# Optimization experiments

Hardware: AMD Instinct MI355X
Metric: run time of the kernel (lower is better)

Reference implementation:

```python
import jax, jax.numpy as jnp
import numpy as np

EPS = 2.220446049250313e-16  # sys.float_info.epsilon
H_BW = 0.1  # bandwidth h


def setup_inputs() -> dict:
    key = jax.random.key(0)
    k1, k2 = jax.random.split(key)
    X = jax.random.normal(k1, (4, 256, 64, 64), dtype=jnp.float32)
    Y = jax.random.normal(k2, (4, 256, 64, 64), dtype=jnp.float32)
    return {"X_features": X, "Y_features": Y}


def _l2_normalize_c(f):
    # torch.norm(f, 2, dim=1, keepdim=True) + eps over channel dim of NCHW
    n = jnp.sqrt(jnp.sum(f * f, axis=1, keepdims=True)) + EPS
    return f / n


def reference(X_features, Y_features):
    B, C = X_features.shape[0], X_features.shape[1]
    # PONO centering: mean over channel dim of Y
    y_mean = jnp.mean(Y_features, axis=1, keepdims=True)  # [B,1,H,W]
    X = X_features - y_mean
    Y = Y_features - y_mean
    Xn = _l2_normalize_c(X).reshape(B, C, -1)  # [B,C,M]
    Yn = _l2_normalize_c(Y).reshape(B, C, -1)  # [B,C,M]
    # cosine distance matrix [B,M,M]
    d = 1.0 - jnp.einsum('bci,bcj->bij', Xn, Yn)
    d_norm = d / (jnp.min(d, axis=-1, keepdims=True) + 0.001)
    w = jnp.exp((1.0 - d_norm) / H_BW)
    A_ij = w / jnp.sum(w, axis=-1, keepdims=True)
    CX = jnp.mean(jnp.max(A_ij, axis=-1), axis=1)  # [B]
    return jnp.mean(-jnp.log(CX))
```

## Files before the change

kernel.cpp:

```cpp
#include <hip/hip_runtime.h>
#include <hip/hip_bf16.h>

typedef unsigned short u16;
typedef unsigned int u32;
typedef __attribute__((ext_vector_type(8))) __bf16 bf16x8;
typedef __attribute__((ext_vector_type(4))) float f32x4;
typedef __attribute__((ext_vector_type(8))) short short8;

#define EPSF 2.220446049250313e-16f

__device__ __forceinline__ u16 f2bf(float f) {
    u32 u = __float_as_uint(f);
    return (u16)((u + 0x7FFFu + ((u >> 16) & 1u)) >> 16);
}

__global__ __launch_bounds__(256) void prep_kernel(
    const float* __restrict__ X, const float* __restrict__ Y,
    u16* __restrict__ Xp, u16* __restrict__ Yp)
{
    const int blk = blockIdx.x;
    const int b = blk >> 8;
    const int fbase = blk & 255;
    const int t = threadIdx.x;
    const int px = t & 15, cg = t >> 4;
    const int l = t & 63, wv = t >> 6;
    const size_t base = (size_t)b * 256 * 4096 + (fbase << 4) + px;

    __shared__ float pA[4][16], pB[4][16];
    __shared__ float meanL[16], rnL[16];

    const int ks = cg >> 1;
    const int g0 = (cg & 1) << 1;
    const size_t pbase = (size_t)b << 20;
    const size_t addr0 = pbase + ((size_t)(fbase * 8 + ks) * 64 + g0 * 16 + px) * 8;

    float vals[16];

    {
        float s1 = 0.f, s2 = 0.f;
        #pragma unroll
        for (int k = 0; k < 16; ++k) {
            float v = Y[base + (size_t)(cg * 16 + k) * 4096];
            vals[k] = v; s1 += v; s2 += v * v;
        }
        s1 += __shfl_xor(s1, 16, 64); s2 += __shfl_xor(s2, 16, 64);
        s1 += __shfl_xor(s1, 32, 64); s2 += __shfl_xor(s2, 32, 64);
        if (l < 16) { pA[wv][l] = s1; pB[wv][l] = s2; }
        __syncthreads();
        if (t < 16) {
            float Sy = pA[0][t] + pA[1][t] + pA[2][t] + pA[3][t];
            float Syy = pB[0][t] + pB[1][t] + pB[2][t] + pB[3][t];
            float m = Sy * (1.f / 256.f);
            meanL[t] = m;
            rnL[t] = 1.f / (sqrtf(fmaxf(Syy - m * Sy, 0.f)) + EPSF);
        }
        __syncthreads();
        float m = meanL[px], rn = rnL[px];
        short8 h0, h1;
        #pragma unroll
        for (int k = 0; k < 8; ++k) {
            h0[k] = (short)f2bf((vals[k] - m) * rn);
            h1[k] = (short)f2bf((vals[8 + k] - m) * rn);
        }
        *(short8*)(Yp + addr0) = h0;
        *(short8*)(Yp + addr0 + 128) = h1;
        __syncthreads();
    }
    {
        float s1 = 0.f, s2 = 0.f;
        #pragma unroll
        for (int k = 0; k < 16; ++k) {
            float v = X[base + (size_t)(cg * 16 + k) * 4096];
            vals[k] = v; s1 += v; s2 += v * v;
        }
        s1 += __shfl_xor(s1, 16, 64); s2 += __shfl_xor(s2, 16, 64);
        s1 += __shfl_xor(s1, 32, 64); s2 += __shfl_xor(s2, 32, 64);
        if (l < 16) { pA[wv][l] = s1; pB[wv][l] = s2; }
        __syncthreads();
        if (t < 16) {
            float Sx = pA[0][t] + pA[1][t] + pA[2][t] + pA[3][t];
            float Sxx = pB[0][t] + pB[1][t] + pB[2][t] + pB[3][t];
            float m = meanL[t];
            rnL[t] = 1.f / (sqrtf(fmaxf(Sxx - 2.f * m * Sx + 256.f * m * m, 0.f)) + EPSF);
        }
        __syncthreads();
        float m = meanL[px], rn = rnL[px];
        short8 h0, h1;
        #pragma unroll
        for (int k = 0; k < 8; ++k) {
            h0[k] = (short)f2bf((vals[k] - m) * rn);
            h1[k] = (short)f2bf((vals[8 + k] - m) * rn);
        }
        *(short8*)(Xp + addr0) = h0;
        *(short8*)(Xp + addr0 + 128) = h1;
    }
}

template <int PASS>
__global__ __launch_bounds__(256, 2) void cx_pass(
    const u16* __restrict__ Xp, const u16* __restrict__ Yp,
    const float* __restrict__ partIn, float* __restrict__ partOut)
{
    __shared__ float smxL[64];
    __shared__ float redL[64][4];

    const int t = threadIdx.x;
    const int w = t >> 6, l = t & 63;
    const int l15 = l & 15, g = l >> 4;
    const int wc = w;

    const int id = blockIdx.x;
    const int xcd = id & 7, slot = id >> 3;
    const int b = xcd >> 1;
    const int it2 = ((xcd & 1) << 5) | (slot >> 1);
    const int jh = slot & 1;
    const int i0 = it2 << 6;

    const size_t pb = (size_t)b << 20;

    if (PASS == 1) {
        if (t < 64) {
            float2 v = ((const float2*)partIn)[(size_t)b * 4096 + i0 + t];
            smxL[t] = fmaxf(v.x, v.y);
        }
        __syncthreads();
    }

    bf16x8 a[4][8];
    {
        const u16* Apl = Xp + pb + (size_t)l * 8;
        #pragma unroll
        for (int fm = 0; fm < 4; ++fm)
            #pragma unroll
            for (int ks = 0; ks < 8; ++ks)
                a[fm][ks] = *(const bf16x8*)(Apl + (size_t)(((i0 >> 4) + fm) * 8 + ks) * 512);
    }

    float mo[4][4], it_[4][4];
    if (PASS == 1) {
        #pragma unroll
        for (int fm = 0; fm < 4; ++fm)
            #pragma unroll
            for (int r = 0; r < 4; ++r) {
                float m = smxL[fm * 16 + g * 4 + r];
                float iv = 14.4269504089f / (1.001f - m);
                it_[fm][r] = iv;
                mo[fm][r] = m * iv;
            }
    }

    float racc[4][4];
    #pragma unroll
    for (int fm = 0; fm < 4; ++fm)
        #pragma unroll
        for (int r = 0; r < 4; ++r) racc[fm][r] = (PASS == 0) ? -2.0f : 0.0f;

    const u16* Bpl = Yp + pb + (size_t)l * 8 + (size_t)(jh * 128 + wc) * 4096;
    #pragma unroll 1
    for (int u = 0; u < 32; ++u) {
        const u16* bp = Bpl + (size_t)u * 16384;
        f32x4 acc0 = {}, acc1 = {}, acc2 = {}, acc3 = {};
        #pragma unroll
        for (int ks = 0; ks < 8; ++ks) {
            bf16x8 bv = *(const bf16x8*)(bp + (ks << 9));
            acc0 = __builtin_amdgcn_mfma_f32_16x16x32_bf16(a[0][ks], bv, acc0, 0, 0, 0);
            acc1 = __builtin_amdgcn_mfma_f32_16x16x32_bf16(a[1][ks], bv, acc1, 0, 0, 0);
            acc2 = __builtin_amdgcn_mfma_f32_16x16x32_bf16(a[2][ks], bv, acc2, 0, 0, 0);
            acc3 = __builtin_amdgcn_mfma_f32_16x16x32_bf16(a[3][ks], bv, acc3, 0, 0, 0);
        }
        if (PASS == 0) {
            #pragma unroll
            for (int r = 0; r < 4; ++r) {
                racc[0][r] = fmaxf(racc[0][r], acc0[r]);
                racc[1][r] = fmaxf(racc[1][r], acc1[r]);
                racc[2][r] = fmaxf(racc[2][r], acc2[r]);
                racc[3][r] = fmaxf(racc[3][r], acc3[r]);
            }
        } else {
            #pragma unroll
            for (int r = 0; r < 4; ++r) {
                racc[0][r] += exp2f(__builtin_fmaf(acc0[r], it_[0][r], -mo[0][r]));
                racc[1][r] += exp2f(__builtin_fmaf(acc1[r], it_[1][r], -mo[1][r]));
                racc[2][r] += exp2f(__builtin_fmaf(acc2[r], it_[2][r], -mo[2][r]));
                racc[3][r] += exp2f(__builtin_fmaf(acc3[r], it_[3][r], -mo[3][r]));
            }
        }
    }

    #pragma unroll
    for (int fm = 0; fm < 4; ++fm)
        #pragma unroll
        for (int r = 0; r < 4; ++r) {
            float v = racc[fm][r];
            if (PASS == 0) {
                v = fmaxf(v, __shfl_xor(v, 1, 64));
                v = fmaxf(v, __shfl_xor(v, 2, 64));
                v = fmaxf(v, __shfl_xor(v, 4, 64));
                v = fmaxf(v, __shfl_xor(v, 8, 64));
            } else {
                v += __shfl_xor(v, 1, 64);
                v += __shfl_xor(v, 2, 64);
                v += __shfl_xor(v, 4, 64);
                v += __shfl_xor(v, 8, 64);
            }
            if (l15 == 0) redL[fm * 16 + g * 4 + r][wc] = v;
        }
    __syncthreads();
    if (t < 64) {
        float4 vv = *(const float4*)&redL[t][0];
        float res = (PASS == 0)
            ? fmaxf(fmaxf(vv.x, vv.y), fmaxf(vv.z, vv.w))
            : (vv.x + vv.y) + (vv.z + vv.w);
        partOut[((size_t)b * 4096 + i0 + t) * 2 + jh] = res;
    }
}

__global__ __launch_bounds__(256) void csum_kernel(
    const float* __restrict__ p1, float* __restrict__ csum)
{
    __shared__ float rr[4];
    const int t = threadIdx.x;
    const int row = blockIdx.x * 256 + t;
    float2 v = ((const float2*)p1)[row];
    float cx = 1.0f / (v.x + v.y);
    #pragma unroll
    for (int sh = 1; sh <= 32; sh <<= 1) cx += __shfl_xor(cx, sh, 64);
    if ((t & 63) == 0) rr[t >> 6] = cx;
    __syncthreads();
    if (t == 0) csum[blockIdx.x] = rr[0] + rr[1] + rr[2] + rr[3];
}

__global__ __launch_bounds__(64) void final_kernel(
    const float* __restrict__ csum, float* __restrict__ out)
{
    __shared__ float rb[4];
    const int t = threadIdx.x;
    float v = csum[t];
    v += __shfl_xor(v, 1, 64);
    v += __shfl_xor(v, 2, 64);
    v += __shfl_xor(v, 4, 64);
    v += __shfl_xor(v, 8, 64);
    if ((t & 15) == 0) rb[t >> 4] = v;
    __syncthreads();
    if (t == 0) {
        float loss = 0.f;
        #pragma unroll
        for (int bb = 0; bb < 4; ++bb)
            loss += -logf(rb[bb] * (1.f / 4096.f));
        out[0] = loss * 0.25f;
    }
}

extern "C" void kernel_launch(void* const* d_in, const int* in_sizes, int n_in,
                              void* d_out, int out_size, void* d_ws, size_t ws_size,
                              hipStream_t stream)
{
    const float* X = (const float*)d_in[0];
    const float* Y = (const float*)d_in[1];
    char* ws = (char*)d_ws;
    u16* Xp = (u16*)(ws);
    u16* Yp = (u16*)(ws + (8u << 20));
    float* part0 = (float*)(ws + (16u << 20));
    float* part1 = (float*)(ws + (16u << 20) + (128u << 10));
    float* csum  = (float*)(ws + (16u << 20) + (256u << 10));
    float* out = (float*)d_out;

    hipLaunchKernelGGL(prep_kernel, dim3(1024), dim3(256), 0, stream,
                       X, Y, Xp, Yp);
    hipLaunchKernelGGL((cx_pass<0>), dim3(512), dim3(256), 0, stream,
                       Xp, Yp, part0, part0);
    hipLaunchKernelGGL((cx_pass<1>), dim3(512), dim3(256), 0, stream,
                       Xp, Yp, part0, part1);
    hipLaunchKernelGGL(csum_kernel, dim3(64), dim3(256), 0, stream,
                       part1, csum);
    hipLaunchKernelGGL(final_kernel, dim3(1), dim3(64), 0, stream,
                       csum, out);
}
```

Before: 169.5 us.

## Shrink cx_pass tiles to 32 rows with 4-way column split; widen prep blocks

The cx_pass kernels now give each block 32 query rows and a quarter of the columns instead of 64 rows and half the columns. That launches 2048 blocks instead of 512, and launch bounds now request 4 blocks per SM, for higher occupancy and better latency hiding. The cost is less A-operand reuse per B load, so more B traffic, and more partial results to merge, with csum and pass 1 reading four partials per row. The prep kernel also moves to 512-thread blocks covering 32 pixels, reducing channel sums through shared memory instead of shuffles.

```diff
diff --git a/kernel.cpp b/kernel.cpp
--- a/kernel.cpp
+++ b/kernel.cpp
@@ -14,53 +14,51 @@
     return (u16)((u + 0x7FFFu + ((u >> 16) & 1u)) >> 16);
 }
 
-__global__ __launch_bounds__(256) void prep_kernel(
+__global__ __launch_bounds__(512) void prep_kernel(
     const float* __restrict__ X, const float* __restrict__ Y,
     u16* __restrict__ Xp, u16* __restrict__ Yp)
 {
     const int blk = blockIdx.x;
-    const int b = blk >> 8;
-    const int fbase = blk & 255;
-    const int t = threadIdx.x;
-    const int px = t & 15, cg = t >> 4;
-    const int l = t & 63, wv = t >> 6;
-    const size_t base = (size_t)b * 256 * 4096 + (fbase << 4) + px;
-
-    __shared__ float pA[4][16], pB[4][16];
-    __shared__ float meanL[16], rnL[16];
-
-    const int ks = cg >> 1;
-    const int g0 = (cg & 1) << 1;
+    const int b = blk >> 7;
+    const int p0 = (blk & 127) << 5;
+    const int t = threadIdx.x;
+    const int pxl = t & 31, cg = t >> 5;
+    const size_t base = (size_t)b * 256 * 4096 + p0 + pxl;
+
+    __shared__ float pS[16][32], pSS[16][32];
+    __shared__ float meanL[32], rnL[32];
+
     const size_t pbase = (size_t)b << 20;
-    const size_t addr0 = pbase + ((size_t)(fbase * 8 + ks) * 64 + g0 * 16 + px) * 8;
+    const int fb = (p0 + pxl) >> 4;
+    const int ks = cg >> 1, g0 = (cg & 1) << 1;
+    const size_t addr0 = pbase + ((size_t)(fb * 8 + ks) * 64 + g0 * 16 + (pxl & 15)) * 8;
 
     float vals[16];
 
     {
         float s1 = 0.f, s2 = 0.f;
         #pragma unroll
-        for (int k = 0; k < 16; ++k) {
-            float v = Y[base + (size_t)(cg * 16 + k) * 4096];
-            vals[k] = v; s1 += v; s2 += v * v;
-        }
-        s1 += __shfl_xor(s1, 16, 64); s2 += __shfl_xor(s2, 16, 64);
-        s1 += __shfl_xor(s1, 32, 64); s2 += __shfl_xor(s2, 32, 64);
-        if (l < 16) { pA[wv][l] = s1; pB[wv][l] = s2; }
-        __syncthreads();
-        if (t < 16) {
-            float Sy = pA[0][t] + pA[1][t] + pA[2][t] + pA[3][t];
-            float Syy = pB[0][t] + pB[1][t] + pB[2][t] + pB[3][t];
+        for (int e = 0; e < 16; ++e) {
+            float v = Y[base + (size_t)(cg * 16 + e) * 4096];
+            vals[e] = v; s1 += v; s2 += v * v;
+        }
+        pS[cg][pxl] = s1; pSS[cg][pxl] = s2;
+        __syncthreads();
+        if (t < 32) {
+            float Sy = 0.f, Syy = 0.f;
+            #pragma unroll
+            for (int c = 0; c < 16; ++c) { Sy += pS[c][t]; Syy += pSS[c][t]; }
             float m = Sy * (1.f / 256.f);
             meanL[t] = m;
             rnL[t] = 1.f / (sqrtf(fmaxf(Syy - m * Sy, 0.f)) + EPSF);
         }
         __syncthreads();
-        float m = meanL[px], rn = rnL[px];
+        const float m = meanL[pxl], rn = rnL[pxl];
         short8 h0, h1;
         #pragma unroll
-        for (int k = 0; k < 8; ++k) {
-            h0[k] = (short)f2bf((vals[k] - m) * rn);
-            h1[k] = (short)f2bf((vals[8 + k] - m) * rn);
+        for (int e = 0; e < 8; ++e) {
+            h0[e] = (short)f2bf((vals[e] - m) * rn);
+            h1[e] = (short)f2bf((vals[8 + e] - m) * rn);
         }
         *(short8*)(Yp + addr0) = h0;
         *(short8*)(Yp + addr0 + 128) = h1;
@@ -69,27 +67,26 @@
     {
         float s1 = 0.f, s2 = 0.f;
         #pragma unroll
-        for (int k = 0; k < 16; ++k) {
-            float v = X[base + (size_t)(cg * 16 + k) * 4096];
-            vals[k] = v; s1 += v; s2 += v * v;
-        }
-        s1 += __shfl_xor(s1, 16, 64); s2 += __shfl_xor(s2, 16, 64);
-        s1 += __shfl_xor(s1, 32, 64); s2 += __shfl_xor(s2, 32, 64);
-        if (l < 16) { pA[wv][l] = s1; pB[wv][l] = s2; }
-        __syncthreads();
-        if (t < 16) {
-            float Sx = pA[0][t] + pA[1][t] + pA[2][t] + pA[3][t];
-            float Sxx = pB[0][t] + pB[1][t] + pB[2][t] + pB[3][t];
+        for (int e = 0; e < 16; ++e) {
+            float v = X[base + (size_t)(cg * 16 + e) * 4096];
+            vals[e] = v; s1 += v; s2 += v * v;
+        }
+        pS[cg][pxl] = s1; pSS[cg][pxl] = s2;
+        __syncthreads();
+        if (t < 32) {
+            float Sx = 0.f, Sxx = 0.f;
+            #pragma unroll
+            for (int c = 0; c < 16; ++c) { Sx += pS[c][t]; Sxx += pSS[c][t]; }
             float m = meanL[t];
             rnL[t] = 1.f / (sqrtf(fmaxf(Sxx - 2.f * m * Sx + 256.f * m * m, 0.f)) + EPSF);
         }
         __syncthreads();
-        float m = meanL[px], rn = rnL[px];
+        const float m = meanL[pxl], rn = rnL[pxl];
         short8 h0, h1;
         #pragma unroll
-        for (int k = 0; k < 8; ++k) {
-            h0[k] = (short)f2bf((vals[k] - m) * rn);
-            h1[k] = (short)f2bf((vals[8 + k] - m) * rn);
+        for (int e = 0; e < 8; ++e) {
+            h0[e] = (short)f2bf((vals[e] - m) * rn);
+            h1[e] = (short)f2bf((vals[8 + e] - m) * rn);
         }
         *(short8*)(Xp + addr0) = h0;
         *(short8*)(Xp + addr0 + 128) = h1;
@@ -97,12 +94,12 @@
 }
 
 template <int PASS>
-__global__ __launch_bounds__(256, 2) void cx_pass(
+__global__ __launch_bounds__(256, 4) void cx_pass(
     const u16* __restrict__ Xp, const u16* __restrict__ Yp,
     const float* __restrict__ partIn, float* __restrict__ partOut)
 {
-    __shared__ float smxL[64];
-    __shared__ float redL[64][4];
+    __shared__ float smxL[32];
+    __shared__ float redL[32][4];
 
     const int t = threadIdx.x;
     const int w = t >> 6, l = t & 63;
@@ -112,34 +109,34 @@
     const int id = blockIdx.x;
     const int xcd = id & 7, slot = id >> 3;
     const int b = xcd >> 1;
-    const int it2 = ((xcd & 1) << 5) | (slot >> 1);
-    const int jh = slot & 1;
-    const int i0 = it2 << 6;
+    const int tl = ((xcd & 1) << 8) | slot;
+    const int it = tl >> 2, jq = tl & 3;
+    const int i0 = it << 5;
 
     const size_t pb = (size_t)b << 20;
 
     if (PASS == 1) {
-        if (t < 64) {
-            float2 v = ((const float2*)partIn)[(size_t)b * 4096 + i0 + t];
-            smxL[t] = fmaxf(v.x, v.y);
-        }
-        __syncthreads();
-    }
-
-    bf16x8 a[4][8];
+        if (t < 32) {
+            float4 v = ((const float4*)partIn)[(size_t)b * 4096 + i0 + t];
+            smxL[t] = fmaxf(fmaxf(v.x, v.y), fmaxf(v.z, v.w));
+        }
+        __syncthreads();
+    }
+
+    bf16x8 a[2][8];
     {
         const u16* Apl = Xp + pb + (size_t)l * 8;
         #pragma unroll
-        for (int fm = 0; fm < 4; ++fm)
+        for (int fm = 0; fm < 2; ++fm)
             #pragma unroll
             for (int ks = 0; ks < 8; ++ks)
                 a[fm][ks] = *(const bf16x8*)(Apl + (size_t)(((i0 >> 4) + fm) * 8 + ks) * 512);
     }
 
-    float mo[4][4], it_[4][4];
+    float mo[2][4], it_[2][4];
     if (PASS == 1) {
         #pragma unroll
-        for (int fm = 0; fm < 4; ++fm)
+        for (int fm = 0; fm < 2; ++fm)
             #pragma unroll
             for (int r = 0; r < 4; ++r) {
                 float m = smxL[fm * 16 + g * 4 + r];
@@ -149,46 +146,40 @@
             }
     }
 
-    float racc[4][4];
+    float racc[2][4];
     #pragma unroll
-    for (int fm = 0; fm < 4; ++fm)
+    for (int fm = 0; fm < 2; ++fm)
         #pragma unroll
         for (int r = 0; r < 4; ++r) racc[fm][r] = (PASS == 0) ? -2.0f : 0.0f;
 
-    const u16* Bpl = Yp + pb + (size_t)l * 8 + (size_t)(jh * 128 + wc) * 4096;
+    const u16* Bpl = Yp + pb + (size_t)l * 8 + (size_t)(jq * 64 + wc) * 4096;
     #pragma unroll 1
-    for (int u = 0; u < 32; ++u) {
+    for (int u = 0; u < 16; ++u) {
         const u16* bp = Bpl + (size_t)u * 16384;
-        f32x4 acc0 = {}, acc1 = {}, acc2 = {}, acc3 = {};
+        f32x4 acc0 = {}, acc1 = {};
         #pragma unroll
         for (int ks = 0; ks < 8; ++ks) {
             bf16x8 bv = *(const bf16x8*)(bp + (ks << 9));
             acc0 = __builtin_amdgcn_mfma_f32_16x16x32_bf16(a[0][ks], bv, acc0, 0, 0, 0);
             acc1 = __builtin_amdgcn_mfma_f32_16x16x32_bf16(a[1][ks], bv, acc1, 0, 0, 0);
-            acc2 = __builtin_amdgcn_mfma_f32_16x16x32_bf16(a[2][ks], bv, acc2, 0, 0, 0);
-            acc3 = __builtin_amdgcn_mfma_f32_16x16x32_bf16(a[3][ks], bv, acc3, 0, 0, 0);
         }
         if (PASS == 0) {
             #pragma unroll
             for (int r = 0; r < 4; ++r) {
                 racc[0][r] = fmaxf(racc[0][r], acc0[r]);
                 racc[1][r] = fmaxf(racc[1][r], acc1[r]);
-                racc[2][r] = fmaxf(racc[2][r], acc2[r]);
-                racc[3][r] = fmaxf(racc[3][r], acc3[r]);
             }
         } else {
             #pragma unroll
             for (int r = 0; r < 4; ++r) {
                 racc[0][r] += exp2f(__builtin_fmaf(acc0[r], it_[0][r], -mo[0][r]));
                 racc[1][r] += exp2f(__builtin_fmaf(acc1[r], it_[1][r], -mo[1][r]));
-                racc[2][r] += exp2f(__builtin_fmaf(acc2[r], it_[2][r], -mo[2][r]));
-                racc[3][r] += exp2f(__builtin_fmaf(acc3[r], it_[3][r], -mo[3][r]));
             }
         }
     }
 
     #pragma unroll
-    for (int fm = 0; fm < 4; ++fm)
+    for (int fm = 0; fm < 2; ++fm)
         #pragma unroll
         for (int r = 0; r < 4; ++r) {
             float v = racc[fm][r];
@@ -206,12 +197,12 @@
             if (l15 == 0) redL[fm * 16 + g * 4 + r][wc] = v;
         }
     __syncthreads();
-    if (t < 64) {
+    if (t < 32) {
         float4 vv = *(const float4*)&redL[t][0];
         float res = (PASS == 0)
             ? fmaxf(fmaxf(vv.x, vv.y), fmaxf(vv.z, vv.w))
             : (vv.x + vv.y) + (vv.z + vv.w);
-        partOut[((size_t)b * 4096 + i0 + t) * 2 + jh] = res;
+        partOut[((size_t)b * 4096 + i0 + t) * 4 + jq] = res;
     }
 }
 
@@ -221,8 +212,8 @@
     __shared__ float rr[4];
     const int t = threadIdx.x;
     const int row = blockIdx.x * 256 + t;
-    float2 v = ((const float2*)p1)[row];
-    float cx = 1.0f / (v.x + v.y);
+    float4 v = ((const float4*)p1)[row];
+    float cx = 1.0f / ((v.x + v.y) + (v.z + v.w));
     #pragma unroll
     for (int sh = 1; sh <= 32; sh <<= 1) cx += __shfl_xor(cx, sh, 64);
     if ((t & 63) == 0) rr[t >> 6] = cx;
@@ -261,15 +252,15 @@
     u16* Xp = (u16*)(ws);
     u16* Yp = (u16*)(ws + (8u << 20));
     float* part0 = (float*)(ws + (16u << 20));
-    float* part1 = (float*)(ws + (16u << 20) + (128u << 10));
-    float* csum  = (float*)(ws + (16u << 20) + (256u << 10));
+    float* part1 = (float*)(ws + (16u << 20) + (256u << 10));
+    float* csum  = (float*)(ws + (16u << 20) + (512u << 10));
     float* out = (float*)d_out;
 
-    hipLaunchKernelGGL(prep_kernel, dim3(1024), dim3(256), 0, stream,
+    hipLaunchKernelGGL(prep_kernel, dim3(512), dim3(512), 0, stream,
                        X, Y, Xp, Yp);
-    hipLaunchKernelGGL((cx_pass<0>), dim3(512), dim3(256), 0, stream,
+    hipLaunchKernelGGL((cx_pass<0>), dim3(2048), dim3(256), 0, stream,
                        Xp, Yp, part0, part0);
-    hipLaunchKernelGGL((cx_pass<1>), dim3(512), dim3(256), 0, stream,
+    hipLaunchKernelGGL((cx_pass<1>), dim3(2048), dim3(256), 0, stream,
                        Xp, Yp, part0, part1);
     hipLaunchKernelGGL(csum_kernel, dim3(64), dim3(256), 0, stream,
                        part1, csum);
```

Result: no change. 168.5 us (-0.5%).
